# Performance work log

Hardware: AMD Instinct MI355X
Metric: run time of the kernel (lower is better)

## Reference

```python
import jax, jax.numpy as jnp
import numpy as np

GAM1 = 1.0
GAM2 = 1.0
EPS = 0.01


def setup_inputs() -> dict:
    key = jax.random.key(0)
    k1, k2 = jax.random.split(key)
    m, p, k = 262144, 128, 10
    x = jax.random.normal(k1, (m, p), dtype=jnp.float32)
    y = jax.random.randint(k2, (m,), 0, k, dtype=jnp.int32)
    return {"x": x, "y": y, "num_classes": k}


def reference(x, y, num_classes):
    m, p = x.shape
    I = jnp.eye(p, dtype=x.dtype)
    scalar = p / (m * EPS)

    # W = x.T, so W @ W.T == x.T @ x  (p x p Gram)
    cov = x.T @ x
    discrimn_empi = jnp.linalg.slogdet(I + GAM1 * scalar * cov)[1] / 2.0
    discrimn_theo = jnp.linalg.slogdet(I + scalar * cov)[1] / 2.0

    # per-class compress loss: logdet(I + p/(n_j*eps) * W_j W_j^T) * n_j / m
    onehot = jax.nn.one_hot(y, num_classes, dtype=x.dtype)  # [m, k]
    counts = onehot.sum(axis=0)                             # [k]

    def class_cov(col):  # col: [m] 0/1 mask for one class
        return (x * col[:, None]).T @ x  # [p, p]

    covs = jax.lax.map(class_cov, onehot.T)  # [k, p, p], sequential over k classes

    safe_counts = jnp.maximum(counts, 1.0)
    scal = p / (safe_counts * EPS)                              # [k]
    lds = jnp.linalg.slogdet(I[None] + scal[:, None, None] * covs)[1]  # [k]
    compress = jnp.sum(jnp.where(counts > 0, lds * counts / m, 0.0)) / 2.0

    total_loss_empi = GAM2 * (-discrimn_empi) + compress
    return total_loss_empi, discrimn_empi, discrimn_theo, compress
```

## Files before the change

### kernel.cpp

```cpp
#include <hip/hip_runtime.h>

#define K 10
#define P 128
#define EPSV 0.01f
#define GAM1 1.0f
#define GAM2 1.0f
#define CH 512
#define SK 64
#define KS 68
#define SORTCH 2048
#define NTHR 256

typedef __attribute__((ext_vector_type(8))) short bf16x8;
typedef __attribute__((ext_vector_type(4))) short s16x4;
typedef __attribute__((ext_vector_type(4))) float f32x4;

static __device__ __forceinline__ short f2bf(float f) {
    unsigned u = __float_as_uint(f);
    u = (u + 0x7FFFu + ((u >> 16) & 1u)) >> 16;
    return (short)u;
}

__global__ void hist_kernel(const int* __restrict__ y, int* __restrict__ blk_counts, int m) {
    __shared__ int h[K];
    int t = threadIdx.x;
    if (t < K) h[t] = 0;
    __syncthreads();
    int base = blockIdx.x * SORTCH;
    int rows = min(SORTCH, m - base);
    for (int i = t; i < rows; i += NTHR) atomicAdd(&h[y[base + i]], 1);
    __syncthreads();
    if (t < K) blk_counts[blockIdx.x * K + t] = h[t];
}

__global__ void scan_kernel(const int* __restrict__ blk_counts, int* __restrict__ blk_offsets,
                            int* __restrict__ counts, int* __restrict__ pstart, int nb) {
    __shared__ int s[K][128];
    __shared__ int sps[K + 1];
    int t = threadIdx.x;
    int own[K];
    if (t < 128) {
        for (int c = 0; c < K; ++c) {
            int v = (t < nb) ? blk_counts[t * K + c] : 0;
            own[c] = v;
            s[c][t] = v;
        }
    }
    __syncthreads();
    for (int off = 1; off < 128; off <<= 1) {
        int tmp[K];
        if (t < 128)
            for (int c = 0; c < K; ++c) tmp[c] = (t >= off) ? s[c][t - off] : 0;
        __syncthreads();
        if (t < 128)
            for (int c = 0; c < K; ++c) s[c][t] += tmp[c];
        __syncthreads();
    }
    if (t == 0) {
        int run = 0;
        for (int c = 0; c < K; ++c) {
            sps[c] = run;
            int tot = s[c][127];
            counts[c] = tot;
            pstart[c] = run;
            run += ((tot + CH - 1) / CH) * CH;
        }
        sps[K] = run;
        pstart[K] = run;
    }
    __syncthreads();
    if (t < nb)
        for (int c = 0; c < K; ++c)
            blk_offsets[t * K + c] = sps[c] + s[c][t] - own[c];
}

__global__ void scatter_kernel(const int* __restrict__ y, const int* __restrict__ blk_offsets,
                               int* __restrict__ perm, int m) {
    __shared__ int cur[K];
    int t = threadIdx.x;
    if (t < K) cur[t] = blk_offsets[blockIdx.x * K + t];
    __syncthreads();
    int base = blockIdx.x * SORTCH;
    int rows = min(SORTCH, m - base);
    for (int i = t; i < rows; i += NTHR) {
        int row = base + i;
        int pos = atomicAdd(&cur[y[row]], 1);
        perm[pos] = row;
    }
}

__global__ __launch_bounds__(NTHR) void gram_kernel(const float* __restrict__ x,
                                                    const int* __restrict__ perm,
                                                    const int* __restrict__ pstart,
                                                    float* __restrict__ grams) {
    __shared__ int pm[CH];
    __shared__ short xsT[P * KS];
    int t = threadIdx.x;
    long base = (long)blockIdx.x * CH;
    int cls = 0;
    for (int c = 1; c < K; ++c)
        if (base >= (long)pstart[c]) cls = c;
    for (int i = t; i < CH; i += NTHR) pm[i] = perm[base + i];

    const int lane = t & 63;
    const int wave = t >> 6;
    const int m16 = lane & 15;
    const int quad = lane >> 4;
    const int wr = wave >> 1;
    const int wc = wave & 1;
    const int c2 = t & 63;
    const int rg = t >> 6;

    f32x4 acc[4][4];
#pragma unroll
    for (int a = 0; a < 4; ++a)
#pragma unroll
        for (int b = 0; b < 4; ++b) acc[a][b] = (f32x4){0.f, 0.f, 0.f, 0.f};

    __syncthreads();

    for (int s = 0; s < CH / SK; ++s) {
        int sb = s * SK;
        float2 v[16];
#pragma unroll
        for (int ii = 0; ii < 16; ++ii) {
            int r = pm[sb + rg * 16 + ii];
            if (r >= 0) v[ii] = ((const float2*)(x + (size_t)r * P))[c2];
            else { v[ii].x = 0.f; v[ii].y = 0.f; }
        }
        __syncthreads();
        short b0[16], b1[16];
#pragma unroll
        for (int ii = 0; ii < 16; ++ii) { b0[ii] = f2bf(v[ii].x); b1[ii] = f2bf(v[ii].y); }
        int col0 = 2 * c2, col1 = 2 * c2 + 1;
#pragma unroll
        for (int q = 0; q < 4; ++q) {
            s16x4 w0 = {b0[q * 4], b0[q * 4 + 1], b0[q * 4 + 2], b0[q * 4 + 3]};
            s16x4 w1 = {b1[q * 4], b1[q * 4 + 1], b1[q * 4 + 2], b1[q * 4 + 3]};
            *(s16x4*)&xsT[col0 * KS + rg * 16 + q * 4] = w0;
            *(s16x4*)&xsT[col1 * KS + rg * 16 + q * 4] = w1;
        }
        __syncthreads();
#pragma unroll
        for (int kk = 0; kk < 2; ++kk) {
            int k0 = kk * 32 + quad * 8;
            bf16x8 af[4], bfr[4];
#pragma unroll
            for (int a = 0; a < 4; ++a) {
                int colA = wr * 64 + a * 16 + m16;
                union { bf16x8 v8; s16x4 h[2]; } u;
                u.h[0] = *(s16x4*)&xsT[colA * KS + k0];
                u.h[1] = *(s16x4*)&xsT[colA * KS + k0 + 4];
                af[a] = u.v8;
            }
#pragma unroll
            for (int b = 0; b < 4; ++b) {
                int colB = wc * 64 + b * 16 + m16;
                union { bf16x8 v8; s16x4 h[2]; } u;
                u.h[0] = *(s16x4*)&xsT[colB * KS + k0];
                u.h[1] = *(s16x4*)&xsT[colB * KS + k0 + 4];
                bfr[b] = u.v8;
            }
#pragma unroll
            for (int a = 0; a < 4; ++a)
#pragma unroll
                for (int b = 0; b < 4; ++b)
                    acc[a][b] = __builtin_amdgcn_mfma_f32_16x16x32_bf16(af[a], bfr[b], acc[a][b], 0, 0, 0);
        }
    }
    float* g = grams + (size_t)cls * P * P;
#pragma unroll
    for (int a = 0; a < 4; ++a)
#pragma unroll
        for (int b = 0; b < 4; ++b)
#pragma unroll
            for (int r = 0; r < 4; ++r) {
                int gi = wr * 64 + a * 16 + quad * 4 + r;
                int gj = wc * 64 + b * 16 + m16;
                if (gi <= gj) atomicAdd(&g[gi * P + gj], acc[a][b][r]);
            }
}

__global__ __launch_bounds__(256) void logdet_kernel(const float* __restrict__ grams,
                                                     const int* __restrict__ counts,
                                                     float* __restrict__ logd, int m) {
    __shared__ float A[P * P];
    int t = threadIdx.x, b = blockIdx.x;
    float scale;
    if (b == 0) scale = GAM1 * (float)P / ((float)m * EPSV);
    else if (b == 1) scale = (float)P / ((float)m * EPSV);
    else {
        float cnt = (float)counts[b - 2];
        if (cnt < 1.f) cnt = 1.f;
        scale = (float)P / (cnt * EPSV);
    }
    for (int idx = t; idx < P * P; idx += 256) {
        int i = idx >> 7, c = idx & (P - 1);
        int src = (i <= c) ? (i * P + c) : (c * P + i);
        float sgm;
        if (b < 2) {
            float ssum = 0.f;
            for (int cc = 0; cc < K; ++cc) ssum += grams[cc * P * P + src];
            sgm = ssum;
        } else {
            sgm = grams[(b - 2) * P * P + src];
        }
        A[idx] = scale * sgm + ((i == c) ? 1.f : 0.f);
    }
    __syncthreads();

    const int lane = t & 63;
    const int wid = t >> 6;
    float lsum = 0.f;

    for (int bs = 0; bs < 4; ++bs) {
        const int j0 = bs * 32;
        if (wid == 0) {
            float a[32];
            if (lane < 32) {
#pragma unroll
                for (int cc = 0; cc < 8; ++cc)
                    *(f32x4*)&a[cc * 4] = *(f32x4*)&A[(j0 + lane) * P + j0 + cc * 4];
            } else {
#pragma unroll
                for (int cc = 0; cc < 32; ++cc) a[cc] = 0.f;
            }
            float myinv = 0.f;
#pragma unroll
            for (int tt = 0; tt < 32; ++tt) {
                float utt = __shfl(a[tt], tt);
                float inv = __builtin_amdgcn_rcpf(utt);
                lsum += __logf(utt);
                if (lane == tt) myinv = inv;
                bool act = (lane < 32) && (lane > tt);
                float lm = act ? a[tt] * inv : 0.f;
                if (act) a[tt] = lm;
#pragma unroll
                for (int k2 = tt + 1; k2 < 32; ++k2) {
                    float utk = __shfl(a[k2], tt);
                    a[k2] -= lm * utk;
                }
            }
            if (lane < 32) A[(j0 + lane) * P + j0 + lane] = myinv;

            if (bs < 3) {
                int nc = P - j0 - 32;
                int c0 = j0 + 32 + lane;
                int c1 = c0 + 64;
                bool v0 = lane < nc;
                bool v1 = lane + 64 < nc;
                int c0a = v0 ? c0 : (j0 + 32);
                int c1a = v1 ? c1 : (j0 + 32);
                float ua[32], ub[32];
#pragma unroll
                for (int j = 0; j < 32; ++j) {
                    float s0 = A[(j0 + j) * P + c0a];
                    float s1 = A[(j0 + j) * P + c1a];
#pragma unroll
                    for (int t2 = 0; t2 < j; ++t2) {
                        float ljt = __shfl(a[t2], j);
                        s0 -= ljt * ua[t2];
                        s1 -= ljt * ub[t2];
                    }
                    ua[j] = s0; ub[j] = s1;
                    if (v0) A[(j0 + j) * P + c0] = s0;
                    if (v1) A[(j0 + j) * P + c1] = s1;
                }
            }
        }
        __syncthreads();

        if (bs < 3) {
            int nc = P - j0 - 32;
            int nt = nc >> 2;
            int ntiles = nt * nt;
            for (int tile = t; tile < ntiles; tile += 256) {
                int ti = tile / nt, tk = tile - ti * nt;
                int i0 = j0 + 32 + ti * 4, k0 = j0 + 32 + tk * 4;
                f32x4 acc0 = {0, 0, 0, 0}, acc1 = {0, 0, 0, 0};
                f32x4 acc2 = {0, 0, 0, 0}, acc3 = {0, 0, 0, 0};
#pragma unroll
                for (int j = 0; j < 32; ++j) {
                    const float* row = &A[(j0 + j) * P];
                    float invd = row[j0 + j];
                    f32x4 ui = *(const f32x4*)&row[i0];
                    f32x4 uk = *(const f32x4*)&row[k0];
                    uk *= invd;
                    acc0 += ui[0] * uk;
                    acc1 += ui[1] * uk;
                    acc2 += ui[2] * uk;
                    acc3 += ui[3] * uk;
                }
                f32x4* r0 = (f32x4*)&A[(i0 + 0) * P + k0];
                f32x4* r1 = (f32x4*)&A[(i0 + 1) * P + k0];
                f32x4* r2 = (f32x4*)&A[(i0 + 2) * P + k0];
                f32x4* r3 = (f32x4*)&A[(i0 + 3) * P + k0];
                *r0 -= acc0; *r1 -= acc1; *r2 -= acc2; *r3 -= acc3;
            }
            __syncthreads();
        }
    }
    if (t == 0) logd[b] = lsum;
}

__global__ void final_kernel(const float* __restrict__ logd, const int* __restrict__ counts,
                             float* __restrict__ out, int m) {
    if (threadIdx.x == 0 && blockIdx.x == 0) {
        float empi = 0.5f * logd[0];
        float theo = 0.5f * logd[1];
        float comp = 0.f;
        for (int c = 0; c < K; ++c) {
            float cnt = (float)counts[c];
            if (cnt > 0.f) comp += logd[2 + c] * cnt / (float)m;
        }
        comp *= 0.5f;
        out[0] = GAM2 * (-empi) + comp;
        out[1] = empi;
        out[2] = theo;
        out[3] = comp;
    }
}

extern "C" void kernel_launch(void* const* d_in, const int* in_sizes, int n_in,
                              void* d_out, int out_size, void* d_ws, size_t ws_size,
                              hipStream_t stream) {
    const float* x = (const float*)d_in[0];
    const int* y = (const int*)d_in[1];
    int m = in_sizes[1];
    int nbs = (m + SORTCH - 1) / SORTCH;
    int nbg = (m + CH - 1) / CH + K;

    char* ws = (char*)d_ws;
    float* grams = (float*)ws;
    float* logd = (float*)(ws + 655360);
    int* counts = (int*)(ws + 655424);
    int* pstart = (int*)(ws + 655488);
    int* blk_counts = (int*)(ws + 655616);
    int* blk_offsets = (int*)(ws + 655616 + (size_t)nbs * K * 4);
    int* perm = (int*)(ws + 655616 + 2 * (size_t)nbs * K * 4);

    hipMemsetAsync(ws, 0, 655488, stream);
    hipMemsetAsync(perm, 0xFF, (size_t)nbg * CH * 4, stream);

    hist_kernel<<<nbs, NTHR, 0, stream>>>(y, blk_counts, m);
    scan_kernel<<<1, NTHR, 0, stream>>>(blk_counts, blk_offsets, counts, pstart, nbs);
    scatter_kernel<<<nbs, NTHR, 0, stream>>>(y, blk_offsets, perm, m);
    gram_kernel<<<nbg, NTHR, 0, stream>>>(x, perm, pstart, grams);
    logdet_kernel<<<K + 2, 256, 0, stream>>>(grams, counts, logd, m);
    final_kernel<<<1, 1, 0, stream>>>(logd, counts, (float*)d_out, m);
}
```

Before: 355.1 us.

## Precompute class-Gram sum in separate kernel and use readlane in logdet panel

Adds a small kernel that sums the per-class Gram matrices once, so the two full-covariance logdet blocks no longer each read all ten class matrices while loading. Inside the panel LU factorization, cross-lane broadcasts from a fixed lane switch from __shfl to v_readlane, avoiding LDS-permute traffic. The triangular solve is split into separate load, compute and store loops so loads can be batched. The trade-offs are an extra kernel launch and higher register pressure from the split loops; launch bounds now state one block per SM.

```diff
diff --git a/kernel.cpp b/kernel.cpp
--- a/kernel.cpp
+++ b/kernel.cpp
@@ -19,6 +19,10 @@
     unsigned u = __float_as_uint(f);
     u = (u + 0x7FFFu + ((u >> 16) & 1u)) >> 16;
     return (short)u;
+}
+
+static __device__ __forceinline__ float rdlane(float v, int srclane) {
+    return __int_as_float(__builtin_amdgcn_readlane(__float_as_int(v), srclane));
 }
 
 __global__ void hist_kernel(const int* __restrict__ y, int* __restrict__ blk_counts, int m) {
@@ -181,9 +185,18 @@
             }
 }
 
-__global__ __launch_bounds__(256) void logdet_kernel(const float* __restrict__ grams,
-                                                     const int* __restrict__ counts,
-                                                     float* __restrict__ logd, int m) {
+__global__ void sum_kernel(const float* __restrict__ grams, float* __restrict__ gsum) {
+    int idx = blockIdx.x * 256 + threadIdx.x;
+    float s = 0.f;
+#pragma unroll
+    for (int c = 0; c < K; ++c) s += grams[c * P * P + idx];
+    gsum[idx] = s;
+}
+
+__global__ __launch_bounds__(256, 1) void logdet_kernel(const float* __restrict__ grams,
+                                                        const float* __restrict__ gsum,
+                                                        const int* __restrict__ counts,
+                                                        float* __restrict__ logd, int m) {
     __shared__ float A[P * P];
     int t = threadIdx.x, b = blockIdx.x;
     float scale;
@@ -194,18 +207,11 @@
         if (cnt < 1.f) cnt = 1.f;
         scale = (float)P / (cnt * EPSV);
     }
+    const float* src = (b < 2) ? gsum : (grams + (size_t)(b - 2) * P * P);
     for (int idx = t; idx < P * P; idx += 256) {
         int i = idx >> 7, c = idx & (P - 1);
-        int src = (i <= c) ? (i * P + c) : (c * P + i);
-        float sgm;
-        if (b < 2) {
-            float ssum = 0.f;
-            for (int cc = 0; cc < K; ++cc) ssum += grams[cc * P * P + src];
-            sgm = ssum;
-        } else {
-            sgm = grams[(b - 2) * P * P + src];
-        }
-        A[idx] = scale * sgm + ((i == c) ? 1.f : 0.f);
+        int s2 = (i <= c) ? idx : (c * P + i);
+        A[idx] = scale * src[s2] + ((i == c) ? 1.f : 0.f);
     }
     __syncthreads();
 
@@ -228,7 +234,7 @@
             float myinv = 0.f;
 #pragma unroll
             for (int tt = 0; tt < 32; ++tt) {
-                float utt = __shfl(a[tt], tt);
+                float utt = rdlane(a[tt], tt);
                 float inv = __builtin_amdgcn_rcpf(utt);
                 lsum += __logf(utt);
                 if (lane == tt) myinv = inv;
@@ -237,7 +243,7 @@
                 if (act) a[tt] = lm;
 #pragma unroll
                 for (int k2 = tt + 1; k2 < 32; ++k2) {
-                    float utk = __shfl(a[k2], tt);
+                    float utk = rdlane(a[k2], tt);
                     a[k2] -= lm * utk;
                 }
             }
@@ -254,17 +260,22 @@
                 float ua[32], ub[32];
 #pragma unroll
                 for (int j = 0; j < 32; ++j) {
-                    float s0 = A[(j0 + j) * P + c0a];
-                    float s1 = A[(j0 + j) * P + c1a];
+                    ua[j] = A[(j0 + j) * P + c0a];
+                    ub[j] = A[(j0 + j) * P + c1a];
+                }
+#pragma unroll
+                for (int j = 0; j < 32; ++j) {
 #pragma unroll
                     for (int t2 = 0; t2 < j; ++t2) {
-                        float ljt = __shfl(a[t2], j);
-                        s0 -= ljt * ua[t2];
-                        s1 -= ljt * ub[t2];
+                        float ljt = rdlane(a[t2], j);
+                        ua[j] -= ljt * ua[t2];
+                        ub[j] -= ljt * ub[t2];
                     }
-                    ua[j] = s0; ub[j] = s1;
-                    if (v0) A[(j0 + j) * P + c0] = s0;
-                    if (v1) A[(j0 + j) * P + c1] = s1;
+                }
+#pragma unroll
+                for (int j = 0; j < 32; ++j) {
+                    if (v0) A[(j0 + j) * P + c0] = ua[j];
+                    if (v1) A[(j0 + j) * P + c1] = ub[j];
                 }
             }
         }
@@ -332,20 +343,22 @@
 
     char* ws = (char*)d_ws;
     float* grams = (float*)ws;
-    float* logd = (float*)(ws + 655360);
-    int* counts = (int*)(ws + 655424);
-    int* pstart = (int*)(ws + 655488);
-    int* blk_counts = (int*)(ws + 655616);
-    int* blk_offsets = (int*)(ws + 655616 + (size_t)nbs * K * 4);
-    int* perm = (int*)(ws + 655616 + 2 * (size_t)nbs * K * 4);
-
-    hipMemsetAsync(ws, 0, 655488, stream);
+    float* gsum = (float*)(ws + 655360);
+    float* logd = (float*)(ws + 720896);
+    int* counts = (int*)(ws + 720960);
+    int* pstart = (int*)(ws + 721024);
+    int* blk_counts = (int*)(ws + 721152);
+    int* blk_offsets = (int*)(ws + 721152 + (size_t)nbs * K * 4);
+    int* perm = (int*)(ws + 721152 + 2 * (size_t)nbs * K * 4);
+
+    hipMemsetAsync(ws, 0, 655360, stream);
     hipMemsetAsync(perm, 0xFF, (size_t)nbg * CH * 4, stream);
 
     hist_kernel<<<nbs, NTHR, 0, stream>>>(y, blk_counts, m);
     scan_kernel<<<1, NTHR, 0, stream>>>(blk_counts, blk_offsets, counts, pstart, nbs);
     scatter_kernel<<<nbs, NTHR, 0, stream>>>(y, blk_offsets, perm, m);
     gram_kernel<<<nbg, NTHR, 0, stream>>>(x, perm, pstart, grams);
-    logdet_kernel<<<K + 2, 256, 0, stream>>>(grams, counts, logd, m);
+    sum_kernel<<<P * P / 256, 256, 0, stream>>>(grams, gsum);
+    logdet_kernel<<<K + 2, 256, 0, stream>>>(grams, gsum, counts, logd, m);
     final_kernel<<<1, 1, 0, stream>>>(logd, counts, (float*)d_out, m);
 }
```

New measurement: 299.5 us. -15.7%, faster.
